# Kernel optimization log

Measured on AMD Instinct MI355X. Metric: run time of the kernel, lower is better.

Reference implementation:

```python
import jax, jax.numpy as jnp
import numpy as np

B, N, F, H1, H2, NC = 1024, 64, 1024, 256, 128, 128
ALPHA = 0.2   # LeakyReLU slope
BN_EPS = 1e-5


def setup_inputs() -> dict:
    key = jax.random.key(0)
    ks = jax.random.split(key, 20)
    d = {}
    d["x"] = jax.random.normal(ks[0], (B, 1, F), dtype=jnp.float32)
    d["neighbor"] = jax.random.normal(ks[1], (B, N, 1, F), dtype=jnp.float32)
    # GraphAttn layer 1 params
    d["W1"] = jax.random.normal(ks[2], (H1, F), dtype=jnp.float32) / np.sqrt(F)
    d["b1"] = jnp.zeros((H1,), dtype=jnp.float32)
    d["a11"] = jax.random.normal(ks[3], (H1,), dtype=jnp.float32) / np.sqrt(H1)
    d["a12"] = jax.random.normal(ks[4], (H1,), dtype=jnp.float32) / np.sqrt(H1)
    d["g1"] = jnp.ones((), dtype=jnp.float32)   # BatchNorm1d(1) weight (scalar)
    d["be1"] = jnp.zeros((), dtype=jnp.float32)  # BatchNorm1d(1) bias
    # GraphAttn layer 2 params
    d["W2"] = jax.random.normal(ks[5], (H2, H1), dtype=jnp.float32) / np.sqrt(H1)
    d["b2"] = jnp.zeros((H2,), dtype=jnp.float32)
    d["a21"] = jax.random.normal(ks[6], (H2,), dtype=jnp.float32) / np.sqrt(H2)
    d["a22"] = jax.random.normal(ks[7], (H2,), dtype=jnp.float32) / np.sqrt(H2)
    d["g2"] = jnp.ones((), dtype=jnp.float32)
    d["be2"] = jnp.zeros((), dtype=jnp.float32)
    # final classifier
    d["Wl"] = jax.random.normal(ks[8], (NC, H2), dtype=jnp.float32) / np.sqrt(H2)
    d["bl"] = jnp.zeros((NC,), dtype=jnp.float32)
    return d


def _l2norm_c(t):
    # torch nf.normalize default: p=2, dim=1 -> here the singleton channel axis (-2)
    n = jnp.sqrt(jnp.sum(t * t, axis=-2, keepdims=True))
    return t / jnp.maximum(n, 1e-12)


def _gat_layer(x, nb, W, b, a_self, a_nb):
    # x: [B,1,Fin], nb: [B,N,1,Fin]
    xh = jnp.einsum('bcf,hf->bch', x, W) + b        # [B,1,H]
    nbh = jnp.einsum('bncf,hf->bnch', nb, W) + b    # [B,N,1,H]
    # att1(x[i]) + att2(neighbor[i]) -> scores over N (C==1 squeezed)
    s = (jnp.einsum('bch,h->bc', xh, a_self)[:, None, :]
         + jnp.einsum('bnch,h->bnc', nbh, a_nb))[..., 0]   # [B,N]
    A = jax.nn.softmax(jax.nn.leaky_relu(s, ALPHA), axis=1)  # softmax over neighbors
    out = jnp.einsum('bn,bnch->bch', A, nbh)        # [B,1,H]
    return out, nbh


def _bn_relu(t, g, b, axes):
    # BatchNorm1d(1) in training mode: stats over all non-channel dims of the tensor
    m = jnp.mean(t, axis=axes, keepdims=True)
    v = jnp.mean(jnp.square(t - m), axis=axes, keepdims=True)
    return jax.nn.relu(g * (t - m) * jax.lax.rsqrt(v + BN_EPS) + b)


def reference(x, neighbor, W1, b1, a11, a12, g1, be1,
              W2, b2, a21, a22, g2, be2, Wl, bl):
    x = _l2norm_c(x)
    nb = _l2norm_c(neighbor)
    x, nb = _gat_layer(x, nb, W1, b1, a11, a12)
    # acvt1 applied to x [B,1,H1] (stats over B,H) and to each neighbor tensor
    # [N,1,H1] separately (per-sample stats -> axes (1,3) of [B,N,1,H1])
    x = _bn_relu(x, g1, be1, axes=(0, 2))
    nb = _bn_relu(nb, g1, be1, axes=(1, 3))
    x, nb = _gat_layer(x, nb, W2, b2, a21, a22)
    x = _bn_relu(x, g2, be2, axes=(0, 2))
    # Flatten -> Dropout(p=0) -> Linear
    logits = jnp.einsum('bh,ch->bc', x.reshape(x.shape[0], -1), Wl) + bl
    return logits
```

## Files before the change

kernel.cpp:

```cpp
#include <hip/hip_runtime.h>
#include <hip/hip_bf16.h>
#include <stdint.h>

#define B_    1024
#define N_    64
#define F_    1024
#define H1_   256
#define H2_   128
#define NC_   128
#define ALPHA 0.2f
#define BN_EPS 1e-5f

typedef __attribute__((ext_vector_type(4))) float  f32x4;
typedef __attribute__((ext_vector_type(8))) __bf16 bf16x8;
typedef __attribute__((ext_vector_type(4))) __bf16 bf16x4;

__device__ inline float sign_ref(float v) {
    float s = copysignf(1.0f, v);
    return (fabsf(v) >= 1e-12f) ? s : v * 1e12f;
}

__device__ __forceinline__ void gload_lds16(const void* g, void* l) {
    auto gp = reinterpret_cast<const __attribute__((address_space(1))) void*>(
        reinterpret_cast<uintptr_t>(g));
    auto lp = reinterpret_cast<__attribute__((address_space(3))) void*>(
        reinterpret_cast<uintptr_t>(l));
    __builtin_amdgcn_global_load_lds(gp, lp, 16, 0, 0);
}

__device__ inline float blk_reduce(float v, float* buf) {
    #pragma unroll
    for (int o = 32; o > 0; o >>= 1) v += __shfl_xor(v, o, 64);
    __syncthreads();
    const int wave = threadIdx.x >> 6, lane = threadIdx.x & 63;
    if (lane == 0) buf[wave] = v;
    __syncthreads();
    float r = 0.f;
    if (threadIdx.x == 0) {
        const int nw = blockDim.x >> 6;
        for (int i = 0; i < nw; ++i) r += buf[i];
    }
    return r;
}

__global__ __launch_bounds__(256) void k_prep(
    const float* __restrict__ W1, const float* __restrict__ W2,
    const float* __restrict__ b1, const float* __restrict__ a11,
    const float* __restrict__ a12, const float* __restrict__ b2,
    const float* __restrict__ a21, const float* __restrict__ a22,
    __bf16* __restrict__ W1b, __bf16* __restrict__ W2b,
    float* __restrict__ w1a, float* __restrict__ w1a12,
    float* __restrict__ w2a, float* __restrict__ w2a22,
    float* __restrict__ cscal)
{
    __shared__ float rbuf[8];
    const int blk = blockIdx.x, tid = threadIdx.x;
    if (blk < 256) {
        const int i0 = blk * 1024 + tid * 4;
        float4 v = *(const float4*)(W1 + i0);
        bf16x4 p = { (__bf16)v.x, (__bf16)v.y, (__bf16)v.z, (__bf16)v.w };
        *(bf16x4*)(W1b + i0) = p;
    } else if (blk < 288) {
        const int i0 = (blk - 256) * 1024 + tid * 4;
        float4 v = *(const float4*)(W2 + i0);
        bf16x4 p = { (__bf16)v.x, (__bf16)v.y, (__bf16)v.z, (__bf16)v.w };
        *(bf16x4*)(W2b + i0) = p;
    } else if (blk < 292) {
        const int f = (blk - 288) * 256 + tid;
        float s1 = 0.f, s2 = 0.f;
        for (int h = 0; h < H1_; ++h) {
            const float w = W1[h * F_ + f];
            s1 += w * a11[h]; s2 += w * a12[h];
        }
        w1a[f] = s1; w1a12[f] = s2;
    } else if (blk == 292) {
        float s1 = 0.f, s2 = 0.f;
        for (int h = 0; h < H2_; ++h) {
            const float w = W2[h * H1_ + tid];
            s1 += w * a21[h]; s2 += w * a22[h];
        }
        w2a[tid] = s1; w2a22[tid] = s2;
    } else {
        float v1 = b1[tid] * a11[tid];
        float v2 = (tid < H2_) ? b2[tid] * a21[tid] : 0.f;
        float v3 = (tid < H2_) ? b2[tid] * a22[tid] : 0.f;
        float r1 = blk_reduce(v1, rbuf);
        float r2 = blk_reduce(v2, rbuf);
        float r3 = blk_reduce(v3, rbuf);
        if (tid == 0) { cscal[0] = r1; cscal[1] = r2; cscal[2] = r3; }
    }
}

__global__ __launch_bounds__(256) void k_sself1(
    const float* __restrict__ x, const float* __restrict__ w1a,
    const float* __restrict__ cscal, float* __restrict__ sself1)
{
    __shared__ float rbuf[8];
    const int b = blockIdx.x, tid = threadIdx.x;
    const float* xb = x + (size_t)b * F_;
    float p = 0.f;
    for (int i = tid; i < F_; i += 256) p += sign_ref(xb[i]) * w1a[i];
    float r = blk_reduce(p, rbuf);
    if (tid == 0) sself1[b] = r + cscal[0];
}

__global__ __launch_bounds__(256, 1) void k_gemm1(
    const float* __restrict__ A, const __bf16* __restrict__ Bw,
    const float* __restrict__ bias, __bf16* __restrict__ C)
{
    constexpr int BM = 128, BN = 256, BK = 64, K = F_;
    constexpr int LDA = BK + 8;
    __shared__ __attribute__((aligned(16))) char smem[BM * LDA * 2 + BN * BK * 2];
    __bf16* As = (__bf16*)smem;
    __bf16* Bs = (__bf16*)(smem + BM * LDA * 2);
    __bf16* Cs = Bs;

    const int tid = threadIdx.x;
    const int wave = tid >> 6, lane = tid & 63;
    const int wm = wave & 1, wn = wave >> 1;
    const int rowin = lane & 15, kq = lane >> 4;
    const size_t m0 = (size_t)blockIdx.x * BM;

    f32x4 acc[4][8] = {};

    const int cqA = tid & 15, r0A = tid >> 4;
    const float* Abase = A + m0 * K + cqA * 4;

    for (int k0 = 0; k0 < K; k0 += BK) {
        #pragma unroll
        for (int it = 0; it < 8; ++it) {
            const int s = it * 256 + tid;
            const int r = s >> 3;
            const int c8 = (s & 7) ^ (r & 7);
            gload_lds16(Bw + (size_t)r * K + k0 + c8 * 8, Bs + s * 8);
        }
        #pragma unroll
        for (int rr = 0; rr < 8; ++rr) {
            const int r = r0A + rr * 16;
            float4 v = *(const float4*)(Abase + (size_t)r * K + k0);
            bf16x4 p = { (__bf16)sign_ref(v.x), (__bf16)sign_ref(v.y),
                         (__bf16)sign_ref(v.z), (__bf16)sign_ref(v.w) };
            *(bf16x4*)&As[r * LDA + cqA * 4] = p;
        }
        __syncthreads();
        #pragma unroll
        for (int ks = 0; ks < 2; ++ks) {
            bf16x8 af[4], bv[8];
            #pragma unroll
            for (int mi = 0; mi < 4; ++mi)
                af[mi] = *(const bf16x8*)&As[(wm * 64 + mi * 16 + rowin) * LDA + ks * 32 + kq * 8];
            #pragma unroll
            for (int ni = 0; ni < 8; ++ni) {
                const int r = wn * 128 + ni * 16 + rowin;
                const int c = (ks * 4 + kq) ^ (r & 7);
                bv[ni] = *(const bf16x8*)&Bs[(r * 8 + c) * 8];
            }
            #pragma unroll
            for (int mi = 0; mi < 4; ++mi)
                #pragma unroll
                for (int ni = 0; ni < 8; ++ni)
                    acc[mi][ni] = __builtin_amdgcn_mfma_f32_16x16x32_bf16(
                        af[mi], bv[ni], acc[mi][ni], 0, 0, 0);
        }
        __syncthreads();
    }
    const int cr0 = (lane >> 4) * 4, cc = lane & 15;
    for (int half = 0; half < 2; ++half) {
        if (wm == half) {
            #pragma unroll
            for (int ni = 0; ni < 8; ++ni) {
                const int col = wn * 128 + ni * 16 + cc;
                const float bs = bias[col];
                #pragma unroll
                for (int mi = 0; mi < 4; ++mi)
                    #pragma unroll
                    for (int i = 0; i < 4; ++i)
                        Cs[(mi * 16 + cr0 + i) * 256 + col] =
                            (__bf16)(acc[mi][ni][i] + bs);
            }
        }
        __syncthreads();
        #pragma unroll
        for (int it = 0; it < 8; ++it) {
            const int s = it * 256 + tid;
            const size_t row = m0 + half * 64 + (s >> 5);
            *(bf16x8*)(C + row * 256 + (s & 31) * 8) = *(const bf16x8*)&Cs[s * 8];
        }
        __syncthreads();
    }
}

__global__ __launch_bounds__(256) void k_agg1(
    const __bf16* __restrict__ nbh1, const float* __restrict__ sself1,
    const float* __restrict__ a12, const float* __restrict__ g1p,
    const float* __restrict__ be1p, float* __restrict__ out1,
    float* __restrict__ alpha1, float* __restrict__ beta1)
{
    __shared__ __attribute__((aligned(16))) __bf16 tile[N_ * H1_];
    __shared__ float a12s[H1_];
    __shared__ float sv[N_];
    __shared__ float rbuf[8];
    const int b = blockIdx.x, tid = threadIdx.x;
    const __bf16* src = nbh1 + (size_t)b * N_ * H1_;
    #pragma unroll
    for (int it = 0; it < 8; ++it)
        ((bf16x8*)tile)[it * 256 + tid] = ((const bf16x8*)src)[it * 256 + tid];
    a12s[tid] = a12[tid];
    __syncthreads();
    {
        const int n = tid >> 2, q = tid & 3;
        float p = 0.f;
        for (int i = 0; i < 64; ++i) {
            const int h = q * 64 + ((i + tid) & 63);
            p += (float)tile[n * H1_ + h] * a12s[h];
        }
        p += __shfl_xor(p, 1); p += __shfl_xor(p, 2);
        if (q == 0) { float s = sself1[b] + p; sv[n] = s > 0.f ? s : ALPHA * s; }
    }
    __syncthreads();
    if (tid < 64) {
        float s = sv[tid], m = s;
        #pragma unroll
        for (int o = 1; o < 64; o <<= 1) m = fmaxf(m, __shfl_xor(m, o));
        float e = __expf(s - m), t = e;
        #pragma unroll
        for (int o = 1; o < 64; o <<= 1) t += __shfl_xor(t, o);
        sv[tid] = e / t;
    }
    __syncthreads();
    float acc = 0.f, ss = 0.f, sq = 0.f;
    for (int n2 = 0; n2 < N_; ++n2) {
        const float v = (float)tile[n2 * H1_ + tid];
        acc += sv[n2] * v; ss += v; sq += v * v;
    }
    out1[(size_t)b * H1_ + tid] = acc;
    const float rs = blk_reduce(ss, rbuf);
    const float rq = blk_reduce(sq, rbuf);
    if (tid == 0) {
        const float inv = 1.f / (float)(N_ * H1_);
        const float mean = rs * inv, var = rq * inv - mean * mean;
        const float a = (*g1p) * rsqrtf(var + BN_EPS);
        alpha1[b] = a; beta1[b] = (*be1p) - a * mean;
    }
}

__global__ __launch_bounds__(256) void k_bnred(
    const float* __restrict__ src, const int n,
    float* __restrict__ psum, float* __restrict__ psq)
{
    __shared__ float rbuf[8];
    float s = 0.f, q = 0.f;
    for (int i = blockIdx.x * 256 + threadIdx.x; i < n; i += 64 * 256) {
        const float v = src[i]; s += v; q += v * v;
    }
    const float rs = blk_reduce(s, rbuf);
    const float rq = blk_reduce(q, rbuf);
    if (threadIdx.x == 0) { psum[blockIdx.x] = rs; psq[blockIdx.x] = rq; }
}

__global__ __launch_bounds__(256) void k_sself2(
    const float* __restrict__ out1, const float* __restrict__ psum,
    const float* __restrict__ psq, const float* __restrict__ gp,
    const float* __restrict__ bep, const float* __restrict__ w2a,
    const float* __restrict__ cscal, float* __restrict__ sself2)
{
    __shared__ float rbuf[8];
    __shared__ float axbx[2];
    const int b = blockIdx.x, tid = threadIdx.x;
    if (tid < 64) {
        float s = psum[tid], q = psq[tid];
        #pragma unroll
        for (int o = 32; o > 0; o >>= 1) { s += __shfl_xor(s, o); q += __shfl_xor(q, o); }
        if (tid == 0) {
            const float n = (float)(B_ * H1_);
            const float mean = s / n, var = q / n - mean * mean;
            const float a = (*gp) * rsqrtf(var + BN_EPS);
            axbx[0] = a; axbx[1] = (*bep) - a * mean;
        }
    }
    __syncthreads();
    const float ax = axbx[0], bx = axbx[1];
    const float v = out1[(size_t)b * H1_ + tid];
    const float x2 = fmaxf(fmaf(ax, v, bx), 0.f);
    float r = blk_reduce(x2 * w2a[tid], rbuf);
    if (tid == 0) sself2[b] = r + cscal[1];
}

__global__ __launch_bounds__(256) void k_agg2(
    const __bf16* __restrict__ nbh1, const float* __restrict__ alpha1,
    const float* __restrict__ beta1, const float* __restrict__ sself2,
    const float* __restrict__ w2a22, const float* __restrict__ cscal,
    const __bf16* __restrict__ W2b, const float* __restrict__ b2,
    float* __restrict__ out2)
{
    __shared__ __attribute__((aligned(16))) __bf16 tile[N_ * H1_];
    __shared__ float wv[H1_];
    __shared__ float sv[N_];
    __shared__ float g2s[H1_ + 8];
    __shared__ float hpart[H2_];
    const int b = blockIdx.x, tid = threadIdx.x;
    const __bf16* src = nbh1 + (size_t)b * N_ * H1_;
    #pragma unroll
    for (int it = 0; it < 8; ++it)
        ((bf16x8*)tile)[it * 256 + tid] = ((const bf16x8*)src)[it * 256 + tid];
    wv[tid] = w2a22[tid];
    const float al = alpha1[b], be = beta1[b];
    __syncthreads();
    {
        const int n = tid >> 2, q = tid & 3;
        float p = 0.f;
        for (int i = 0; i < 64; ++i) {
            const int h = q * 64 + ((i + tid) & 63);
            const float v = (float)tile[n * H1_ + h];
            p += fmaxf(fmaf(al, v, be), 0.f) * wv[h];
        }
        p += __shfl_xor(p, 1); p += __shfl_xor(p, 2);
        if (q == 0) {
            float s = sself2[b] + p + cscal[2];
            sv[n] = s > 0.f ? s : ALPHA * s;
        }
    }
    __syncthreads();
    if (tid < 64) {
        float s = sv[tid], m = s;
        #pragma unroll
        for (int o = 1; o < 64; o <<= 1) m = fmaxf(m, __shfl_xor(m, o));
        float e = __expf(s - m), t = e;
        #pragma unroll
        for (int o = 1; o < 64; o <<= 1) t += __shfl_xor(t, o);
        sv[tid] = e / t;
    }
    __syncthreads();
    {
        float g = 0.f;
        for (int n2 = 0; n2 < N_; ++n2) {
            const float v = (float)tile[n2 * H1_ + tid];
            g += sv[n2] * fmaxf(fmaf(al, v, be), 0.f);
        }
        g2s[tid + (tid >> 5)] = g;
    }
    __syncthreads();
    #pragma unroll 4
    for (int j = 0; j < 16; ++j) {
        const int idx = j * 256 + tid;
        const int h = idx >> 5, k8 = idx & 31;
        const bf16x8 w = ((const bf16x8*)W2b)[idx];
        float p = 0.f;
        #pragma unroll
        for (int i = 0; i < 8; ++i) {
            const int k = k8 * 8 + i;
            p += (float)w[i] * g2s[k + (k >> 5)];
        }
        p += __shfl_xor(p, 1); p += __shfl_xor(p, 2); p += __shfl_xor(p, 4);
        p += __shfl_xor(p, 8); p += __shfl_xor(p, 16);
        if ((tid & 31) == 0) hpart[h] = p;
    }
    __syncthreads();
    if (tid < H2_) out2[(size_t)b * H2_ + tid] = hpart[tid] + b2[tid];
}

__global__ __launch_bounds__(128) void k_final(
    const float* __restrict__ out2, const float* __restrict__ psum,
    const float* __restrict__ psq, const float* __restrict__ gp,
    const float* __restrict__ bep, const float* __restrict__ Wl,
    const float* __restrict__ bl, float* __restrict__ logits)
{
    __shared__ float xr[H2_];
    __shared__ float Ws[NC_][H2_ + 1];
    __shared__ float axbx[2];
    const int b = blockIdx.x, tid = threadIdx.x;
    if (tid < 64) {
        float s = psum[tid], q = psq[tid];
        #pragma unroll
        for (int o = 32; o > 0; o >>= 1) { s += __shfl_xor(s, o); q += __shfl_xor(q, o); }
        if (tid == 0) {
            const float n = (float)(B_ * H2_);
            const float mean = s / n, var = q / n - mean * mean;
            const float a = (*gp) * rsqrtf(var + BN_EPS);
            axbx[0] = a; axbx[1] = (*bep) - a * mean;
        }
    }
    for (int i = tid; i < NC_ * H2_ / 4; i += 128) {
        float4 v = ((const float4*)Wl)[i];
        const int r = i >> 5, c = (i & 31) * 4;
        Ws[r][c] = v.x; Ws[r][c + 1] = v.y; Ws[r][c + 2] = v.z; Ws[r][c + 3] = v.w;
    }
    __syncthreads();
    xr[tid] = fmaxf(fmaf(axbx[0], out2[(size_t)b * H2_ + tid], axbx[1]), 0.f);
    __syncthreads();
    float acc = bl[tid];
    #pragma unroll 4
    for (int h = 0; h < H2_; ++h) acc += xr[h] * Ws[tid][h];
    logits[(size_t)b * NC_ + tid] = acc;
}

extern "C" void kernel_launch(void* const* d_in, const int* in_sizes, int n_in,
                              void* d_out, int out_size, void* d_ws, size_t ws_size,
                              hipStream_t stream)
{
    const float* x   = (const float*)d_in[0];
    const float* nb  = (const float*)d_in[1];
    const float* W1  = (const float*)d_in[2];
    const float* b1  = (const float*)d_in[3];
    const float* a11 = (const float*)d_in[4];
    const float* a12 = (const float*)d_in[5];
    const float* g1  = (const float*)d_in[6];
    const float* be1 = (const float*)d_in[7];
    const float* W2  = (const float*)d_in[8];
    const float* b2  = (const float*)d_in[9];
    const float* a21 = (const float*)d_in[10];
    const float* a22 = (const float*)d_in[11];
    const float* g2  = (const float*)d_in[12];
    const float* be2 = (const float*)d_in[13];
    const float* Wl  = (const float*)d_in[14];
    const float* bl  = (const float*)d_in[15];
    float* logits = (float*)d_out;

    size_t off = 0;
    auto alc = [&](size_t bytes) {
        void* p = (char*)d_ws + off;
        off = (off + bytes + 255) & ~(size_t)255;
        return p;
    };
    __bf16* W1b   = (__bf16*)alc((size_t)H1_ * F_ * 2);
    __bf16* W2b   = (__bf16*)alc((size_t)H2_ * H1_ * 2);
    float* w1a    = (float*)alc(F_ * 4);
    float* w1a12  = (float*)alc(F_ * 4);
    float* w2a    = (float*)alc(H1_ * 4);
    float* w2a22  = (float*)alc(H1_ * 4);
    float* cscal  = (float*)alc(3 * 4);
    float* sself1 = (float*)alc(B_ * 4);
    float* sself2 = (float*)alc(B_ * 4);
    float* alpha1 = (float*)alc(B_ * 4);
    float* beta1  = (float*)alc(B_ * 4);
    float* psum1  = (float*)alc(64 * 4);
    float* psq1   = (float*)alc(64 * 4);
    float* psum2  = (float*)alc(64 * 4);
    float* psq2   = (float*)alc(64 * 4);
    float* out1   = (float*)alc((size_t)B_ * H1_ * 4);
    float* out2   = (float*)alc((size_t)B_ * H2_ * 4);
    __bf16* nbh1  = (__bf16*)alc((size_t)B_ * N_ * H1_ * 2);

    k_prep<<<294, 256, 0, stream>>>(W1, W2, b1, a11, a12, b2, a21, a22,
                                    W1b, W2b, w1a, w1a12, w2a, w2a22, cscal);
    k_sself1<<<B_, 256, 0, stream>>>(x, w1a, cscal, sself1);
    k_gemm1<<<(B_ * N_) / 128, 256, 0, stream>>>(nb, W1b, b1, nbh1);
    k_agg1<<<B_, 256, 0, stream>>>(nbh1, sself1, a12, g1, be1, out1, alpha1, beta1);
    k_bnred<<<64, 256, 0, stream>>>(out1, B_ * H1_, psum1, psq1);
    k_sself2<<<B_, 256, 0, stream>>>(out1, psum1, psq1, g1, be1, w2a, cscal, sself2);
    k_agg2<<<B_, 256, 0, stream>>>(nbh1, alpha1, beta1, sself2, w2a22, cscal,
                                   W2b, b2, out2);
    k_bnred<<<64, 256, 0, stream>>>(out2, B_ * H2_, psum2, psq2);
    k_final<<<B_, 128, 0, stream>>>(out2, psum2, psq2, g2, be2, Wl, bl, logits);
}
```

Before: 501.5 us.

## Fuse layer-1 attention, aggregation and BN stats into GEMM epilogue; atomic BN sums

Folds the self-score dot product and the full layer-1 attention softmax/aggregation into the GEMM1 epilogue, reusing the output tile held in LDS instead of rereading nbh1 in a separate kernel. The global BatchNorm sums are accumulated with atomics, replacing the k_bnred passes, and the self-score for layer 2 moves into k_agg2. Kernel launches drop from nine to four, and an extra pass over nbh1 plus the two reduction kernels go away. In exchange the GEMM epilogue does more serial work at one block per CU, and float atomics make the BN sums order-nondeterministic.

```diff
diff --git a/kernel.cpp b/kernel.cpp
--- a/kernel.cpp
+++ b/kernel.cpp
@@ -46,12 +46,12 @@
 __global__ __launch_bounds__(256) void k_prep(
     const float* __restrict__ W1, const float* __restrict__ W2,
     const float* __restrict__ b1, const float* __restrict__ a11,
-    const float* __restrict__ a12, const float* __restrict__ b2,
-    const float* __restrict__ a21, const float* __restrict__ a22,
+    const float* __restrict__ b2, const float* __restrict__ a21,
+    const float* __restrict__ a22,
     __bf16* __restrict__ W1b, __bf16* __restrict__ W2b,
-    float* __restrict__ w1a, float* __restrict__ w1a12,
-    float* __restrict__ w2a, float* __restrict__ w2a22,
-    float* __restrict__ cscal)
+    float* __restrict__ w1a, float* __restrict__ w2a,
+    float* __restrict__ w2a22, float* __restrict__ cscal,
+    float* __restrict__ gsum)
 {
     __shared__ float rbuf[8];
     const int blk = blockIdx.x, tid = threadIdx.x;
@@ -67,12 +67,9 @@
         *(bf16x4*)(W2b + i0) = p;
     } else if (blk < 292) {
         const int f = (blk - 288) * 256 + tid;
-        float s1 = 0.f, s2 = 0.f;
-        for (int h = 0; h < H1_; ++h) {
-            const float w = W1[h * F_ + f];
-            s1 += w * a11[h]; s2 += w * a12[h];
-        }
-        w1a[f] = s1; w1a12[f] = s2;
+        float s1 = 0.f;
+        for (int h = 0; h < H1_; ++h) s1 += W1[h * F_ + f] * a11[h];
+        w1a[f] = s1;
     } else if (blk == 292) {
         float s1 = 0.f, s2 = 0.f;
         for (int h = 0; h < H2_; ++h) {
@@ -87,26 +84,22 @@
         float r1 = blk_reduce(v1, rbuf);
         float r2 = blk_reduce(v2, rbuf);
         float r3 = blk_reduce(v3, rbuf);
-        if (tid == 0) { cscal[0] = r1; cscal[1] = r2; cscal[2] = r3; }
-    }
-}
-
-__global__ __launch_bounds__(256) void k_sself1(
-    const float* __restrict__ x, const float* __restrict__ w1a,
-    const float* __restrict__ cscal, float* __restrict__ sself1)
-{
-    __shared__ float rbuf[8];
-    const int b = blockIdx.x, tid = threadIdx.x;
-    const float* xb = x + (size_t)b * F_;
-    float p = 0.f;
-    for (int i = tid; i < F_; i += 256) p += sign_ref(xb[i]) * w1a[i];
-    float r = blk_reduce(p, rbuf);
-    if (tid == 0) sself1[b] = r + cscal[0];
+        if (tid == 0) {
+            cscal[0] = r1; cscal[1] = r2; cscal[2] = r3;
+            gsum[0] = 0.f; gsum[1] = 0.f; gsum[2] = 0.f; gsum[3] = 0.f;
+        }
+    }
 }
 
 __global__ __launch_bounds__(256, 1) void k_gemm1(
     const float* __restrict__ A, const __bf16* __restrict__ Bw,
-    const float* __restrict__ bias, __bf16* __restrict__ C)
+    const float* __restrict__ bias,
+    const float* __restrict__ x, const float* __restrict__ w1a,
+    const float* __restrict__ a12, const float* __restrict__ cscal,
+    const float* __restrict__ g1p, const float* __restrict__ be1p,
+    __bf16* __restrict__ C, float* __restrict__ out1,
+    float* __restrict__ alpha1, float* __restrict__ beta1,
+    float* __restrict__ gsum)
 {
     constexpr int BM = 128, BN = 256, BK = 64, K = F_;
     constexpr int LDA = BK + 8;
@@ -114,6 +107,10 @@
     __bf16* As = (__bf16*)smem;
     __bf16* Bs = (__bf16*)(smem + BM * LDA * 2);
     __bf16* Cs = Bs;
+    __shared__ float a12s[H1_];
+    __shared__ float sv[N_];
+    __shared__ float rbuf[8];
+    __shared__ float sselfs[2];
 
     const int tid = threadIdx.x;
     const int wave = tid >> 6, lane = tid & 63;
@@ -121,8 +118,22 @@
     const int rowin = lane & 15, kq = lane >> 4;
     const size_t m0 = (size_t)blockIdx.x * BM;
 
+    a12s[tid] = a12[tid];
+    {
+        const float4 wv = *(const float4*)(w1a + tid * 4);
+        const float c1 = cscal[0];
+        #pragma unroll
+        for (int h = 0; h < 2; ++h) {
+            const int b = blockIdx.x * 2 + h;
+            float4 xv = *(const float4*)(x + (size_t)b * F_ + tid * 4);
+            float p = sign_ref(xv.x) * wv.x + sign_ref(xv.y) * wv.y
+                    + sign_ref(xv.z) * wv.z + sign_ref(xv.w) * wv.w;
+            float r = blk_reduce(p, rbuf);
+            if (tid == 0) sselfs[h] = r + c1;
+        }
+    }
+
     f32x4 acc[4][8] = {};
-
     const int cqA = tid & 15, r0A = tid >> 4;
     const float* Abase = A + m0 * K + cqA * 4;
 
@@ -164,8 +175,11 @@
         }
         __syncthreads();
     }
+
+    const float gg = *g1p, bb1 = *be1p;
     const int cr0 = (lane >> 4) * 4, cc = lane & 15;
     for (int half = 0; half < 2; ++half) {
+        const int b = blockIdx.x * 2 + half;
         if (wm == half) {
             #pragma unroll
             for (int ni = 0; ni < 8; ++ni) {
@@ -186,126 +200,92 @@
             const size_t row = m0 + half * 64 + (s >> 5);
             *(bf16x8*)(C + row * 256 + (s & 31) * 8) = *(const bf16x8*)&Cs[s * 8];
         }
-        __syncthreads();
-    }
-}
-
-__global__ __launch_bounds__(256) void k_agg1(
-    const __bf16* __restrict__ nbh1, const float* __restrict__ sself1,
-    const float* __restrict__ a12, const float* __restrict__ g1p,
-    const float* __restrict__ be1p, float* __restrict__ out1,
-    float* __restrict__ alpha1, float* __restrict__ beta1)
+        float ss = 0.f, sq = 0.f;
+        {
+            const int n = tid >> 2, q = tid & 3;
+            float p = 0.f;
+            for (int i = 0; i < 64; ++i) {
+                const int h = q * 64 + ((i + tid) & 63);
+                const float v = (float)Cs[n * H1_ + h];
+                p += v * a12s[h];
+                ss += v; sq += v * v;
+            }
+            p += __shfl_xor(p, 1); p += __shfl_xor(p, 2);
+            if (q == 0) {
+                float s = sselfs[half] + p;
+                sv[n] = s > 0.f ? s : ALPHA * s;
+            }
+        }
+        const float rs = blk_reduce(ss, rbuf);
+        const float rq = blk_reduce(sq, rbuf);
+        if (tid == 0) {
+            const float inv = 1.f / (float)(N_ * H1_);
+            const float mean = rs * inv, var = rq * inv - mean * mean;
+            const float a = gg * rsqrtf(var + BN_EPS);
+            alpha1[b] = a; beta1[b] = bb1 - a * mean;
+        }
+        __syncthreads();
+        if (tid < 64) {
+            float s = sv[tid], m = s;
+            #pragma unroll
+            for (int o = 1; o < 64; o <<= 1) m = fmaxf(m, __shfl_xor(m, o));
+            float e = __expf(s - m), t = e;
+            #pragma unroll
+            for (int o = 1; o < 64; o <<= 1) t += __shfl_xor(t, o);
+            sv[tid] = e / t;
+        }
+        __syncthreads();
+        {
+            float o = 0.f;
+            for (int n2 = 0; n2 < N_; ++n2)
+                o += sv[n2] * (float)Cs[n2 * H1_ + tid];
+            out1[(size_t)b * H1_ + tid] = o;
+            float r1 = blk_reduce(o, rbuf);
+            float r2 = blk_reduce(o * o, rbuf);
+            if (tid == 0) { atomicAdd(&gsum[0], r1); atomicAdd(&gsum[1], r2); }
+        }
+        __syncthreads();
+    }
+}
+
+__global__ __launch_bounds__(256) void k_agg2(
+    const __bf16* __restrict__ nbh1, const float* __restrict__ alpha1,
+    const float* __restrict__ beta1, const float* __restrict__ out1,
+    const float* __restrict__ gsum, const float* __restrict__ g1p,
+    const float* __restrict__ be1p, const float* __restrict__ w2a,
+    const float* __restrict__ w2a22, const float* __restrict__ cscal,
+    const __bf16* __restrict__ W2b, const float* __restrict__ b2,
+    float* __restrict__ out2, float* __restrict__ gsum2)
 {
     __shared__ __attribute__((aligned(16))) __bf16 tile[N_ * H1_];
-    __shared__ float a12s[H1_];
-    __shared__ float sv[N_];
-    __shared__ float rbuf[8];
-    const int b = blockIdx.x, tid = threadIdx.x;
-    const __bf16* src = nbh1 + (size_t)b * N_ * H1_;
-    #pragma unroll
-    for (int it = 0; it < 8; ++it)
-        ((bf16x8*)tile)[it * 256 + tid] = ((const bf16x8*)src)[it * 256 + tid];
-    a12s[tid] = a12[tid];
-    __syncthreads();
-    {
-        const int n = tid >> 2, q = tid & 3;
-        float p = 0.f;
-        for (int i = 0; i < 64; ++i) {
-            const int h = q * 64 + ((i + tid) & 63);
-            p += (float)tile[n * H1_ + h] * a12s[h];
-        }
-        p += __shfl_xor(p, 1); p += __shfl_xor(p, 2);
-        if (q == 0) { float s = sself1[b] + p; sv[n] = s > 0.f ? s : ALPHA * s; }
-    }
-    __syncthreads();
-    if (tid < 64) {
-        float s = sv[tid], m = s;
-        #pragma unroll
-        for (int o = 1; o < 64; o <<= 1) m = fmaxf(m, __shfl_xor(m, o));
-        float e = __expf(s - m), t = e;
-        #pragma unroll
-        for (int o = 1; o < 64; o <<= 1) t += __shfl_xor(t, o);
-        sv[tid] = e / t;
-    }
-    __syncthreads();
-    float acc = 0.f, ss = 0.f, sq = 0.f;
-    for (int n2 = 0; n2 < N_; ++n2) {
-        const float v = (float)tile[n2 * H1_ + tid];
-        acc += sv[n2] * v; ss += v; sq += v * v;
-    }
-    out1[(size_t)b * H1_ + tid] = acc;
-    const float rs = blk_reduce(ss, rbuf);
-    const float rq = blk_reduce(sq, rbuf);
-    if (tid == 0) {
-        const float inv = 1.f / (float)(N_ * H1_);
-        const float mean = rs * inv, var = rq * inv - mean * mean;
-        const float a = (*g1p) * rsqrtf(var + BN_EPS);
-        alpha1[b] = a; beta1[b] = (*be1p) - a * mean;
-    }
-}
-
-__global__ __launch_bounds__(256) void k_bnred(
-    const float* __restrict__ src, const int n,
-    float* __restrict__ psum, float* __restrict__ psq)
-{
-    __shared__ float rbuf[8];
-    float s = 0.f, q = 0.f;
-    for (int i = blockIdx.x * 256 + threadIdx.x; i < n; i += 64 * 256) {
-        const float v = src[i]; s += v; q += v * v;
-    }
-    const float rs = blk_reduce(s, rbuf);
-    const float rq = blk_reduce(q, rbuf);
-    if (threadIdx.x == 0) { psum[blockIdx.x] = rs; psq[blockIdx.x] = rq; }
-}
-
-__global__ __launch_bounds__(256) void k_sself2(
-    const float* __restrict__ out1, const float* __restrict__ psum,
-    const float* __restrict__ psq, const float* __restrict__ gp,
-    const float* __restrict__ bep, const float* __restrict__ w2a,
-    const float* __restrict__ cscal, float* __restrict__ sself2)
-{
-    __shared__ float rbuf[8];
-    __shared__ float axbx[2];
-    const int b = blockIdx.x, tid = threadIdx.x;
-    if (tid < 64) {
-        float s = psum[tid], q = psq[tid];
-        #pragma unroll
-        for (int o = 32; o > 0; o >>= 1) { s += __shfl_xor(s, o); q += __shfl_xor(q, o); }
-        if (tid == 0) {
-            const float n = (float)(B_ * H1_);
-            const float mean = s / n, var = q / n - mean * mean;
-            const float a = (*gp) * rsqrtf(var + BN_EPS);
-            axbx[0] = a; axbx[1] = (*bep) - a * mean;
-        }
-    }
-    __syncthreads();
-    const float ax = axbx[0], bx = axbx[1];
-    const float v = out1[(size_t)b * H1_ + tid];
-    const float x2 = fmaxf(fmaf(ax, v, bx), 0.f);
-    float r = blk_reduce(x2 * w2a[tid], rbuf);
-    if (tid == 0) sself2[b] = r + cscal[1];
-}
-
-__global__ __launch_bounds__(256) void k_agg2(
-    const __bf16* __restrict__ nbh1, const float* __restrict__ alpha1,
-    const float* __restrict__ beta1, const float* __restrict__ sself2,
-    const float* __restrict__ w2a22, const float* __restrict__ cscal,
-    const __bf16* __restrict__ W2b, const float* __restrict__ b2,
-    float* __restrict__ out2)
-{
-    __shared__ __attribute__((aligned(16))) __bf16 tile[N_ * H1_];
-    __shared__ float wv[H1_];
+    __shared__ float wv[H1_], w2as[H1_];
     __shared__ float sv[N_];
     __shared__ float g2s[H1_ + 8];
     __shared__ float hpart[H2_];
+    __shared__ float rbuf[8];
+    __shared__ float sc[3];
     const int b = blockIdx.x, tid = threadIdx.x;
     const __bf16* src = nbh1 + (size_t)b * N_ * H1_;
     #pragma unroll
     for (int it = 0; it < 8; ++it)
         ((bf16x8*)tile)[it * 256 + tid] = ((const bf16x8*)src)[it * 256 + tid];
     wv[tid] = w2a22[tid];
+    w2as[tid] = w2a[tid];
+    if (tid == 0) {
+        const float n = (float)(B_ * H1_);
+        const float mean = gsum[0] / n, var = gsum[1] / n - mean * mean;
+        const float a = (*g1p) * rsqrtf(var + BN_EPS);
+        sc[0] = a; sc[1] = (*be1p) - a * mean;
+    }
+    __syncthreads();
+    {
+        const float v = out1[(size_t)b * H1_ + tid];
+        const float x2 = fmaxf(fmaf(sc[0], v, sc[1]), 0.f);
+        float r = blk_reduce(x2 * w2as[tid], rbuf);
+        if (tid == 0) sc[2] = r + cscal[1];
+    }
+    __syncthreads();
     const float al = alpha1[b], be = beta1[b];
-    __syncthreads();
     {
         const int n = tid >> 2, q = tid & 3;
         float p = 0.f;
@@ -316,7 +296,7 @@
         }
         p += __shfl_xor(p, 1); p += __shfl_xor(p, 2);
         if (q == 0) {
-            float s = sself2[b] + p + cscal[2];
+            float s = sc[2] + p + cscal[2];
             sv[n] = s > 0.f ? s : ALPHA * s;
         }
     }
@@ -356,29 +336,31 @@
         if ((tid & 31) == 0) hpart[h] = p;
     }
     __syncthreads();
-    if (tid < H2_) out2[(size_t)b * H2_ + tid] = hpart[tid] + b2[tid];
+    float o = 0.f;
+    if (tid < H2_) {
+        o = hpart[tid] + b2[tid];
+        out2[(size_t)b * H2_ + tid] = o;
+    }
+    float r1 = blk_reduce(o, rbuf);
+    float r2 = blk_reduce(o * o, rbuf);
+    if (tid == 0) { atomicAdd(&gsum2[0], r1); atomicAdd(&gsum2[1], r2); }
 }
 
 __global__ __launch_bounds__(128) void k_final(
-    const float* __restrict__ out2, const float* __restrict__ psum,
-    const float* __restrict__ psq, const float* __restrict__ gp,
-    const float* __restrict__ bep, const float* __restrict__ Wl,
-    const float* __restrict__ bl, float* __restrict__ logits)
+    const float* __restrict__ out2, const float* __restrict__ gsum2,
+    const float* __restrict__ gp, const float* __restrict__ bep,
+    const float* __restrict__ Wl, const float* __restrict__ bl,
+    float* __restrict__ logits)
 {
     __shared__ float xr[H2_];
     __shared__ float Ws[NC_][H2_ + 1];
     __shared__ float axbx[2];
     const int b = blockIdx.x, tid = threadIdx.x;
-    if (tid < 64) {
-        float s = psum[tid], q = psq[tid];
-        #pragma unroll
-        for (int o = 32; o > 0; o >>= 1) { s += __shfl_xor(s, o); q += __shfl_xor(q, o); }
-        if (tid == 0) {
-            const float n = (float)(B_ * H2_);
-            const float mean = s / n, var = q / n - mean * mean;
-            const float a = (*gp) * rsqrtf(var + BN_EPS);
-            axbx[0] = a; axbx[1] = (*bep) - a * mean;
-        }
+    if (tid == 0) {
+        const float n = (float)(B_ * H2_);
+        const float mean = gsum2[0] / n, var = gsum2[1] / n - mean * mean;
+        const float a = (*gp) * rsqrtf(var + BN_EPS);
+        axbx[0] = a; axbx[1] = (*bep) - a * mean;
     }
     for (int i = tid; i < NC_ * H2_ / 4; i += 128) {
         float4 v = ((const float4*)Wl)[i];
@@ -425,31 +407,22 @@
     __bf16* W1b   = (__bf16*)alc((size_t)H1_ * F_ * 2);
     __bf16* W2b   = (__bf16*)alc((size_t)H2_ * H1_ * 2);
     float* w1a    = (float*)alc(F_ * 4);
-    float* w1a12  = (float*)alc(F_ * 4);
     float* w2a    = (float*)alc(H1_ * 4);
     float* w2a22  = (float*)alc(H1_ * 4);
     float* cscal  = (float*)alc(3 * 4);
-    float* sself1 = (float*)alc(B_ * 4);
-    float* sself2 = (float*)alc(B_ * 4);
+    float* gsum   = (float*)alc(4 * 4);
     float* alpha1 = (float*)alc(B_ * 4);
     float* beta1  = (float*)alc(B_ * 4);
-    float* psum1  = (float*)alc(64 * 4);
-    float* psq1   = (float*)alc(64 * 4);
-    float* psum2  = (float*)alc(64 * 4);
-    float* psq2   = (float*)alc(64 * 4);
     float* out1   = (float*)alc((size_t)B_ * H1_ * 4);
     float* out2   = (float*)alc((size_t)B_ * H2_ * 4);
     __bf16* nbh1  = (__bf16*)alc((size_t)B_ * N_ * H1_ * 2);
 
-    k_prep<<<294, 256, 0, stream>>>(W1, W2, b1, a11, a12, b2, a21, a22,
-                                    W1b, W2b, w1a, w1a12, w2a, w2a22, cscal);
-    k_sself1<<<B_, 256, 0, stream>>>(x, w1a, cscal, sself1);
-    k_gemm1<<<(B_ * N_) / 128, 256, 0, stream>>>(nb, W1b, b1, nbh1);
-    k_agg1<<<B_, 256, 0, stream>>>(nbh1, sself1, a12, g1, be1, out1, alpha1, beta1);
-    k_bnred<<<64, 256, 0, stream>>>(out1, B_ * H1_, psum1, psq1);
-    k_sself2<<<B_, 256, 0, stream>>>(out1, psum1, psq1, g1, be1, w2a, cscal, sself2);
-    k_agg2<<<B_, 256, 0, stream>>>(nbh1, alpha1, beta1, sself2, w2a22, cscal,
-                                   W2b, b2, out2);
-    k_bnred<<<64, 256, 0, stream>>>(out2, B_ * H2_, psum2, psq2);
-    k_final<<<B_, 128, 0, stream>>>(out2, psum2, psq2, g2, be2, Wl, bl, logits);
-}
+    k_prep<<<294, 256, 0, stream>>>(W1, W2, b1, a11, b2, a21, a22,
+                                    W1b, W2b, w1a, w2a, w2a22, cscal, gsum);
+    k_gemm1<<<(B_ * N_) / 128, 256, 0, stream>>>(
+        nb, W1b, b1, x, w1a, a12, cscal, g1, be1,
+        nbh1, out1, alpha1, beta1, gsum);
+    k_agg2<<<B_, 256, 0, stream>>>(nbh1, alpha1, beta1, out1, gsum, g1, be1,
+                                   w2a, w2a22, cscal, W2b, b2, out2, gsum + 2);
+    k_final<<<B_, 128, 0, stream>>>(out2, gsum + 2, g2, be2, Wl, bl, logits);
+}
```

Result: slower. 534.3 us (+6.6%).
